# Kernel optimization log

Hardware: AMD Instinct MI355X
Metric: run time of the kernel (lower is better)

## Reference

```python
import jax, jax.numpy as jnp
import numpy as np

EPS_BN = 1e-5      # torch BatchNorm2d default eps
EPSILON = 1e-12    # signed-sqrt eps from the module
K = 3              # hardcoded k in forward


def _knn_idx(f, k):
    # f: [B, C, N] -> idx [B, N, k] of nearest neighbors (largest -dist^2)
    xx = jnp.sum(f * f, axis=1)                      # [B, N]
    inner = jnp.einsum('bcn,bcm->bnm', f, f)         # [B, N, N]
    pd = -xx[:, :, None] + 2.0 * inner - xx[:, None, :]
    return jax.lax.top_k(pd, k)[1]                   # [B, N, k]


def _graph_feature(f, k):
    # f: [B, C, N] -> [B, N, k, 2C] = concat(neighbor - center, center)
    idx = _knn_idx(f, k)
    ft = jnp.transpose(f, (0, 2, 1))                 # [B, N, C]
    neigh = jax.vmap(lambda x, i: x[i])(ft, idx)     # [B, N, k, C]
    center = jnp.broadcast_to(ft[:, :, None, :], neigh.shape)
    return jnp.concatenate([neigh - center, center], axis=-1)


def _edgeconv(f, W, gamma, beta, mean, var, k):
    # f: [B, C, N]; W: [O, 2C] (1x1 conv, no bias); eval-mode BN; LeakyReLU(0.2); max over k
    g = _graph_feature(f, k)                         # [B, N, k, 2C]
    y = jnp.einsum('bnkc,oc->bonk', g, W)            # [B, O, N, k]
    scale = (gamma / jnp.sqrt(var + EPS_BN))[None, :, None, None]
    y = (y - mean[None, :, None, None]) * scale + beta[None, :, None, None]
    y = jnp.where(y >= 0, y, 0.2 * y)                # LeakyReLU(0.2)
    return jnp.max(y, axis=-1)                       # [B, O, N]


def setup_inputs() -> dict:
    key = jax.random.key(0)
    ks = jax.random.split(key, 12)
    B, C, H, W, M = 64, 768, 26, 26, 32
    inp = {
        'features': jax.random.normal(ks[0], (B, C, H, W), jnp.float32),
        'attentions': jax.random.uniform(ks[1], (B, M, H, W), jnp.float32),
        'W1': jax.random.normal(ks[2], (C, 2 * C), jnp.float32) * 0.02,
        'gamma1': jax.random.uniform(ks[3], (C,), jnp.float32, 0.5, 1.5),
        'beta1': jax.random.normal(ks[4], (C,), jnp.float32) * 0.1,
        'mean1': jax.random.normal(ks[5], (C,), jnp.float32) * 0.1,
        'var1': jax.random.uniform(ks[6], (C,), jnp.float32, 0.5, 1.5),
        'W2': jax.random.normal(ks[7], (C, 2 * C), jnp.float32) * 0.02,
        'gamma2': jax.random.uniform(ks[8], (C,), jnp.float32, 0.5, 1.5),
        'beta2': jax.random.normal(ks[9], (C,), jnp.float32) * 0.1,
        'mean2': jax.random.normal(ks[10], (C,), jnp.float32) * 0.1,
        'var2': jax.random.uniform(ks[11], (C,), jnp.float32, 0.5, 1.5),
    }
    return inp


def reference(features, attentions, W1, gamma1, beta1, mean1, var1,
              W2, gamma2, beta2, mean2, var2):
    B = features.shape[0]
    # AdaptiveMaxPool2d(1) of features * attn_m, per attention map m.
    # lax.map over M avoids materializing the [B, M, C, H, W] product.
    def per_m(attn_m):                                # attn_m: [B, H, W]
        return jnp.max(features * attn_m[:, None, :, :], axis=(2, 3))  # [B, C]
    fm = jax.lax.map(per_m, jnp.transpose(attentions, (1, 0, 2, 3)))   # [M, B, C]
    fm = jnp.transpose(fm, (1, 2, 0))                 # [B, C, M]

    f1 = _edgeconv(fm, W1, gamma1, beta1, mean1, var1, K)   # [B, C, M]
    f2 = _edgeconv(f1, W2, gamma2, beta2, mean2, var2, K)   # [B, C, M]

    fuse = jnp.concatenate([f1, f2], axis=1).reshape(B, -1)  # [B, 2C*M]
    fuse = jnp.sign(fuse) * jnp.sqrt(jnp.abs(fuse) + EPSILON)
    norm = jnp.maximum(jnp.linalg.norm(fuse, axis=-1, keepdims=True), 1e-12)
    return fuse / norm
```

## Files before the change

kernel.cpp:

```cpp
#include <hip/hip_runtime.h>
#include <cfloat>
#include <cmath>

#define B_    64
#define C_    768
#define HW_   676
#define M_    32
#define TWOC_ 1536

__global__ __launch_bounds__(256) void pool_kernel(
    const float* __restrict__ feat, const float* __restrict__ attn,
    float* __restrict__ fm)
{
    const int b      = blockIdx.x / 12;
    const int cchunk = blockIdx.x % 12;
    const int t  = threadIdx.x;
    const int cl = t >> 2;
    const int m0 = (t & 3) * 8;
    const int c  = cchunk * 64 + cl;

    __shared__ float a_s[64][32];

    float acc[8];
#pragma unroll
    for (int j = 0; j < 8; ++j) acc[j] = -FLT_MAX;

    const float* fp = feat + ((size_t)b * C_ + c) * HW_;
    const float* ap = attn + (size_t)b * M_ * HW_;

    for (int hw0 = 0; hw0 < HW_; hw0 += 64) {
        const int hwlen = min(64, HW_ - hw0);
        __syncthreads();
        for (int idx = t; idx < 64 * 32; idx += 256) {
            int hw = idx >> 5, m = idx & 31;
            if (hw < hwlen) a_s[hw][m] = ap[m * HW_ + hw0 + hw];
        }
        __syncthreads();
        for (int hw = 0; hw < hwlen; hw += 4) {
            float4 f4 = *(const float4*)(fp + hw0 + hw);
            float fv[4] = {f4.x, f4.y, f4.z, f4.w};
#pragma unroll
            for (int q = 0; q < 4; ++q) {
                float f = fv[q];
#pragma unroll
                for (int j = 0; j < 8; ++j) {
                    float p = __fmul_rn(f, a_s[hw + q][m0 + j]);
                    acc[j] = fmaxf(acc[j], p);
                }
            }
        }
    }
    float* op = fm + ((size_t)b * C_ + c) * M_ + m0;
#pragma unroll
    for (int j = 0; j < 8; ++j) op[j] = acc[j];
}

__global__ __launch_bounds__(1024) void knn_kernel(
    const float* __restrict__ X, int* __restrict__ idxout)
{
    const int b = blockIdx.x;
    const int t = threadIdx.x;
    const int n = t >> 5, m = t & 31;

    __shared__ float xs[96][32];
    __shared__ float GF[32][32];
    __shared__ float G2[32][32];
    __shared__ float XS[32];
    __shared__ float XP[32];
    __shared__ float PA[32][32], PC[32][32], PDm[32][32];

    const float* Xb = X + (size_t)b * (C_ * M_);
    float accF = 0.f;
    float accP0 = 0.f, accP1 = 0.f;
    float accXs = 0.f;
    float leaf[8];

#pragma unroll
    for (int chunk = 0; chunk < 8; ++chunk) {
        __syncthreads();
        for (int i = t; i < 96 * 32; i += 1024)
            xs[i >> 5][i & 31] = Xb[(size_t)(chunk * 96 + (i >> 5)) * M_ + (i & 31)];
        __syncthreads();
#pragma unroll
        for (int c = 0; c < 96; ++c)
            accF = __fmaf_rn(xs[c][n], xs[c][m], accF);
        if (chunk < 4) {
#pragma unroll
            for (int c = 0; c < 96; ++c)
                accP0 = __fmaf_rn(xs[c][n], xs[c][m], accP0);
        } else {
#pragma unroll
            for (int c = 0; c < 96; ++c)
                accP1 = __fmaf_rn(xs[c][n], xs[c][m], accP1);
        }
        if (t < 32) {
#pragma unroll
            for (int c = 0; c < 96; ++c) {
                float v = xs[c][m];
                accXs = __fadd_rn(accXs, __fmul_rn(v, v));
            }
            float r[8];
#pragma unroll
            for (int j = 0; j < 8; ++j) {
                float v = xs[j][m];
                r[j] = __fmul_rn(v, v);
            }
            for (int i = 8; i < 96; i += 8) {
#pragma unroll
                for (int j = 0; j < 8; ++j) {
                    float v = xs[i + j][m];
                    r[j] = __fadd_rn(r[j], __fmul_rn(v, v));
                }
            }
            leaf[chunk] = __fadd_rn(
                __fadd_rn(__fadd_rn(r[0], r[1]), __fadd_rn(r[2], r[3])),
                __fadd_rn(__fadd_rn(r[4], r[5]), __fadd_rn(r[6], r[7])));
        }
    }
    GF[n][m] = accF;
    G2[n][m] = __fadd_rn(accP0, accP1);
    if (t < 32) {
        XS[m] = accXs;
        XP[m] = __fadd_rn(
            __fadd_rn(__fadd_rn(leaf[0], leaf[1]), __fadd_rn(leaf[2], leaf[3])),
            __fadd_rn(__fadd_rn(leaf[4], leaf[5]), __fadd_rn(leaf[6], leaf[7])));
    }
    __syncthreads();
    PA[n][m]  = __fsub_rn(__fadd_rn(-XS[n], 2.0f * GF[n][m]), XS[m]);
    PC[n][m]  = __fsub_rn(__fadd_rn(-XP[n], 2.0f * G2[n][m]), XP[m]);
    PDm[n][m] = __fsub_rn(__fadd_rn(-XP[n], 2.0f * GF[n][m]), XP[m]);
    __syncthreads();

    if (t < 32) {
        const int nn = t;
        const float* pa = PA[nn];
        const float* pc = PC[nn];
        const float* pd = PDm[nn];

        unsigned masks[3] = {0u, 0u, 0u};
        const float* rows[3] = {pa, pc, pd};
#pragma unroll
        for (int s = 0; s < 3; ++s) {
            unsigned chosen = 0;
            for (int p = 0; p < 3; ++p) {
                float best = -FLT_MAX; int bi = 0;
                for (int mm = 0; mm < 32; ++mm) {
                    if (chosen & (1u << mm)) continue;
                    float v = rows[s][mm];
                    if (v > best) { best = v; bi = mm; }
                }
                chosen |= 1u << bi;
            }
            masks[s] = chosen;
        }
        const unsigned mA = masks[0], mC = masks[1], mD = masks[2];

        unsigned chosen = 0;
        for (int p = 0; p < 3; ++p) {
            int bv = -1; float bp = -FLT_MAX; int bi = 0;
            for (int mm = 0; mm < 32; ++mm) {
                if (chosen & (1u << mm)) continue;
                int v = (int)((mA >> mm) & 1u) + (int)((mC >> mm) & 1u)
                      + (int)((mD >> mm) & 1u);
                float q = pd[mm];
                if (v > bv || (v == bv && q > bp)) { bv = v; bp = q; bi = mm; }
            }
            chosen |= 1u << bi;
            idxout[((size_t)b * 32 + nn) * 3 + p] = bi;
        }
    }
}

__global__ __launch_bounds__(256) void conv_kernel(
    const float* __restrict__ X, const float* __restrict__ W,
    const int* __restrict__ idx,
    const float* __restrict__ gamma, const float* __restrict__ beta,
    const float* __restrict__ mean,  const float* __restrict__ var,
    float* __restrict__ fout)
{
    const int b  = blockIdx.x / 12;
    const int oT = blockIdx.x % 12;
    const int o0 = oT * 64;
    const int t  = threadIdx.x;
    const int oG = t >> 4;
    const int nkg = t & 15;

    __shared__ float fs[C_ * M_];
    __shared__ int   idx_s[M_ * 3];

    const float* Xb = X + (size_t)b * (C_ * M_);
    for (int i = t; i < (C_ * M_) / 4; i += 256)
        ((float4*)fs)[i] = ((const float4*)Xb)[i];
    if (t < 96) idx_s[t] = idx[b * 96 + t];
    __syncthreads();

    const int n_0 = nkg * 2;
    int nn_[6], jj[6];
#pragma unroll
    for (int q = 0; q < 6; ++q) {
        nn_[q] = n_0 + (q >= 3 ? 1 : 0);
        jj[q]  = idx_s[nn_[q] * 3 + (q % 3)];
    }

    const float* Wr0 = W + (size_t)(o0 + oG * 4 + 0) * TWOC_;
    const float* Wr1 = W + (size_t)(o0 + oG * 4 + 1) * TWOC_;
    const float* Wr2 = W + (size_t)(o0 + oG * 4 + 2) * TWOC_;
    const float* Wr3 = W + (size_t)(o0 + oG * 4 + 3) * TWOC_;

    float A[4][6], Bv[4][6], Cv[4][6], Dv[4][6];

    auto sweep = [&](int lane, float (&OUT)[4][6]) {
#pragma unroll
        for (int i = 0; i < 4; ++i)
#pragma unroll
            for (int q = 0; q < 6; ++q) OUT[i][q] = 0.f;
        for (int c = lane; c < C_; c += 8) {
            float w0 = Wr0[c], w1 = Wr1[c], w2 = Wr2[c], w3 = Wr3[c];
            float g[6];
#pragma unroll
            for (int q = 0; q < 6; ++q)
                g[q] = __fsub_rn(fs[c * 32 + jj[q]], fs[c * 32 + nn_[q]]);
#pragma unroll
            for (int q = 0; q < 6; ++q) {
                OUT[0][q] = __fmaf_rn(w0, g[q], OUT[0][q]);
                OUT[1][q] = __fmaf_rn(w1, g[q], OUT[1][q]);
                OUT[2][q] = __fmaf_rn(w2, g[q], OUT[2][q]);
                OUT[3][q] = __fmaf_rn(w3, g[q], OUT[3][q]);
            }
        }
        for (int c = C_ + lane; c < TWOC_; c += 8) {
            float w0 = Wr0[c], w1 = Wr1[c], w2 = Wr2[c], w3 = Wr3[c];
            float g[6];
#pragma unroll
            for (int q = 0; q < 6; ++q)
                g[q] = fs[(c - C_) * 32 + nn_[q]];
#pragma unroll
            for (int q = 0; q < 6; ++q) {
                OUT[0][q] = __fmaf_rn(w0, g[q], OUT[0][q]);
                OUT[1][q] = __fmaf_rn(w1, g[q], OUT[1][q]);
                OUT[2][q] = __fmaf_rn(w2, g[q], OUT[2][q]);
                OUT[3][q] = __fmaf_rn(w3, g[q], OUT[3][q]);
            }
        }
    };
    auto add24 = [&](float (&Xa)[4][6], float (&Ya)[4][6]) {
#pragma unroll
        for (int i = 0; i < 4; ++i)
#pragma unroll
            for (int q = 0; q < 6; ++q)
                Xa[i][q] = __fadd_rn(Xa[i][q], Ya[i][q]);
    };

    sweep(0, A);  sweep(4, Bv); add24(A, Bv);
    sweep(2, Bv); sweep(6, Cv); add24(Bv, Cv);
    add24(A, Bv);
    sweep(1, Bv); sweep(5, Cv); add24(Bv, Cv);
    sweep(3, Cv); sweep(7, Dv); add24(Cv, Dv);
    add24(Bv, Cv);
    add24(A, Bv);

#pragma unroll
    for (int i = 0; i < 4; ++i) {
        const int o = o0 + oG * 4 + i;
        const float sc = __fdiv_rn(gamma[o], __fsqrt_rn(__fadd_rn(var[o], 1e-5f)));
        const float mu = mean[o], be = beta[o];
#pragma unroll
        for (int nl = 0; nl < 2; ++nl) {
            float r = -FLT_MAX;
#pragma unroll
            for (int k = 0; k < 3; ++k) {
                float y = A[i][nl * 3 + k];
                y = __fadd_rn(__fmul_rn(__fsub_rn(y, mu), sc), be);
                y = (y >= 0.f) ? y : __fmul_rn(0.2f, y);
                r = fmaxf(r, y);
            }
            fout[((size_t)b * C_ + o) * M_ + (n_0 + nl)] = r;
        }
    }
}

__global__ __launch_bounds__(256) void fuse_kernel(
    const float* __restrict__ f1, const float* __restrict__ f2,
    float* __restrict__ out)
{
    const int b = blockIdx.x;
    const int t = threadIdx.x;
    const float* p1 = f1 + (size_t)b * (C_ * M_);
    const float* p2 = f2 + (size_t)b * (C_ * M_);
    float* po = out + (size_t)b * (2 * C_ * M_);

    __shared__ double red[256];

    double lsum = 0.0;
    for (int i = t; i < 2 * C_ * M_; i += 256) {
        float x = (i < C_ * M_) ? p1[i] : p2[i - C_ * M_];
        float sq = __fsqrt_rn(__fadd_rn(fabsf(x), 1e-12f));
        float s = (x > 0.f) ? sq : ((x < 0.f) ? -sq : 0.f);
        lsum += (double)s * (double)s;
    }
    red[t] = lsum;
    __syncthreads();
    for (int off = 128; off > 0; off >>= 1) {
        if (t < off) red[t] += red[t + off];
        __syncthreads();
    }
    const float normf = fmaxf((float)sqrt(red[0]), 1e-12f);
    for (int i = t; i < 2 * C_ * M_; i += 256) {
        float x = (i < C_ * M_) ? p1[i] : p2[i - C_ * M_];
        float sq = __fsqrt_rn(__fadd_rn(fabsf(x), 1e-12f));
        float s = (x > 0.f) ? sq : ((x < 0.f) ? -sq : 0.f);
        po[i] = __fdiv_rn(s, normf);
    }
}

extern "C" void kernel_launch(void* const* d_in, const int* in_sizes, int n_in,
                              void* d_out, int out_size, void* d_ws, size_t ws_size,
                              hipStream_t stream)
{
    const float* feat = (const float*)d_in[0];
    const float* attn = (const float*)d_in[1];
    const float* W1   = (const float*)d_in[2];
    const float* g1   = (const float*)d_in[3];
    const float* be1  = (const float*)d_in[4];
    const float* mu1  = (const float*)d_in[5];
    const float* va1  = (const float*)d_in[6];
    const float* W2   = (const float*)d_in[7];
    const float* g2   = (const float*)d_in[8];
    const float* be2  = (const float*)d_in[9];
    const float* mu2  = (const float*)d_in[10];
    const float* va2  = (const float*)d_in[11];

    const size_t FM = (size_t)B_ * C_ * M_;
    float* fm  = (float*)d_ws;
    float* f1  = fm + FM;
    float* f2  = f1 + FM;
    int* idx1  = (int*)(f2 + FM);
    int* idx2  = idx1 + B_ * M_ * 3;

    pool_kernel<<<dim3(768), dim3(256), 0, stream>>>(feat, attn, fm);
    knn_kernel<<<dim3(64), dim3(1024), 0, stream>>>(fm, idx1);
    conv_kernel<<<dim3(768), dim3(256), 0, stream>>>(fm, W1, idx1, g1, be1, mu1, va1, f1);
    knn_kernel<<<dim3(64), dim3(1024), 0, stream>>>(f1, idx2);
    conv_kernel<<<dim3(768), dim3(256), 0, stream>>>(f1, W2, idx2, g2, be2, mu2, va2, f2);
    fuse_kernel<<<dim3(64), dim3(256), 0, stream>>>(f1, f2, (float*)d_out);
}
```

Measured before the change: 1.396 ms.

## Map one output channel per thread in conv kernel with 1024-thread blocks

The edge-conv kernel moves from 256-thread blocks, where each thread accumulated four output channels, to 1024-thread blocks where each thread computes a single output channel for its pair of points. Because the 96 KB shared feature tile allows only one block per CU, this raises the number of waves per CU so memory and LDS latency can be hidden better. In exchange, each gathered feature difference read from shared memory now feeds one FMA instead of four. That quadruples LDS traffic per FMA and also multiplies redundant weight loads.

```diff
diff --git a/kernel.cpp b/kernel.cpp
--- a/kernel.cpp
+++ b/kernel.cpp
@@ -171,7 +171,7 @@
     }
 }
 
-__global__ __launch_bounds__(256) void conv_kernel(
+__global__ __launch_bounds__(1024, 4) void conv_kernel(
     const float* __restrict__ X, const float* __restrict__ W,
     const int* __restrict__ idx,
     const float* __restrict__ gamma, const float* __restrict__ beta,
@@ -189,7 +189,7 @@
     __shared__ int   idx_s[M_ * 3];
 
     const float* Xb = X + (size_t)b * (C_ * M_);
-    for (int i = t; i < (C_ * M_) / 4; i += 256)
+    for (int i = t; i < (C_ * M_) / 4; i += 1024)
         ((float4*)fs)[i] = ((const float4*)Xb)[i];
     if (t < 96) idx_s[t] = idx[b * 96 + t];
     __syncthreads();
@@ -202,80 +202,58 @@
         jj[q]  = idx_s[nn_[q] * 3 + (q % 3)];
     }
 
-    const float* Wr0 = W + (size_t)(o0 + oG * 4 + 0) * TWOC_;
-    const float* Wr1 = W + (size_t)(o0 + oG * 4 + 1) * TWOC_;
-    const float* Wr2 = W + (size_t)(o0 + oG * 4 + 2) * TWOC_;
-    const float* Wr3 = W + (size_t)(o0 + oG * 4 + 3) * TWOC_;
-
-    float A[4][6], Bv[4][6], Cv[4][6], Dv[4][6];
-
-    auto sweep = [&](int lane, float (&OUT)[4][6]) {
-#pragma unroll
-        for (int i = 0; i < 4; ++i)
-#pragma unroll
-            for (int q = 0; q < 6; ++q) OUT[i][q] = 0.f;
+    const int o = o0 + oG;
+    const float* Wr = W + (size_t)o * TWOC_;
+
+    float A[6], Bv[6], Cv[6], Dv[6];
+
+    auto sweep = [&](int lane, float (&OUT)[6]) {
+#pragma unroll
+        for (int q = 0; q < 6; ++q) OUT[q] = 0.f;
         for (int c = lane; c < C_; c += 8) {
-            float w0 = Wr0[c], w1 = Wr1[c], w2 = Wr2[c], w3 = Wr3[c];
-            float g[6];
-#pragma unroll
-            for (int q = 0; q < 6; ++q)
-                g[q] = __fsub_rn(fs[c * 32 + jj[q]], fs[c * 32 + nn_[q]]);
+            float w = Wr[c];
 #pragma unroll
             for (int q = 0; q < 6; ++q) {
-                OUT[0][q] = __fmaf_rn(w0, g[q], OUT[0][q]);
-                OUT[1][q] = __fmaf_rn(w1, g[q], OUT[1][q]);
-                OUT[2][q] = __fmaf_rn(w2, g[q], OUT[2][q]);
-                OUT[3][q] = __fmaf_rn(w3, g[q], OUT[3][q]);
+                float g = __fsub_rn(fs[c * 32 + jj[q]], fs[c * 32 + nn_[q]]);
+                OUT[q] = __fmaf_rn(w, g, OUT[q]);
             }
         }
         for (int c = C_ + lane; c < TWOC_; c += 8) {
-            float w0 = Wr0[c], w1 = Wr1[c], w2 = Wr2[c], w3 = Wr3[c];
-            float g[6];
-#pragma unroll
-            for (int q = 0; q < 6; ++q)
-                g[q] = fs[(c - C_) * 32 + nn_[q]];
+            float w = Wr[c];
 #pragma unroll
             for (int q = 0; q < 6; ++q) {
-                OUT[0][q] = __fmaf_rn(w0, g[q], OUT[0][q]);
-                OUT[1][q] = __fmaf_rn(w1, g[q], OUT[1][q]);
-                OUT[2][q] = __fmaf_rn(w2, g[q], OUT[2][q]);
-                OUT[3][q] = __fmaf_rn(w3, g[q], OUT[3][q]);
+                float g = fs[(c - C_) * 32 + nn_[q]];
+                OUT[q] = __fmaf_rn(w, g, OUT[q]);
             }
         }
     };
-    auto add24 = [&](float (&Xa)[4][6], float (&Ya)[4][6]) {
-#pragma unroll
-        for (int i = 0; i < 4; ++i)
-#pragma unroll
-            for (int q = 0; q < 6; ++q)
-                Xa[i][q] = __fadd_rn(Xa[i][q], Ya[i][q]);
+    auto add6 = [&](float (&Xa)[6], float (&Ya)[6]) {
+#pragma unroll
+        for (int q = 0; q < 6; ++q)
+            Xa[q] = __fadd_rn(Xa[q], Ya[q]);
     };
 
-    sweep(0, A);  sweep(4, Bv); add24(A, Bv);
-    sweep(2, Bv); sweep(6, Cv); add24(Bv, Cv);
-    add24(A, Bv);
-    sweep(1, Bv); sweep(5, Cv); add24(Bv, Cv);
-    sweep(3, Cv); sweep(7, Dv); add24(Cv, Dv);
-    add24(Bv, Cv);
-    add24(A, Bv);
-
-#pragma unroll
-    for (int i = 0; i < 4; ++i) {
-        const int o = o0 + oG * 4 + i;
-        const float sc = __fdiv_rn(gamma[o], __fsqrt_rn(__fadd_rn(var[o], 1e-5f)));
-        const float mu = mean[o], be = beta[o];
-#pragma unroll
-        for (int nl = 0; nl < 2; ++nl) {
-            float r = -FLT_MAX;
-#pragma unroll
-            for (int k = 0; k < 3; ++k) {
-                float y = A[i][nl * 3 + k];
-                y = __fadd_rn(__fmul_rn(__fsub_rn(y, mu), sc), be);
-                y = (y >= 0.f) ? y : __fmul_rn(0.2f, y);
-                r = fmaxf(r, y);
-            }
-            fout[((size_t)b * C_ + o) * M_ + (n_0 + nl)] = r;
-        }
+    sweep(0, A);  sweep(4, Bv); add6(A, Bv);
+    sweep(2, Bv); sweep(6, Cv); add6(Bv, Cv);
+    add6(A, Bv);
+    sweep(1, Bv); sweep(5, Cv); add6(Bv, Cv);
+    sweep(3, Cv); sweep(7, Dv); add6(Cv, Dv);
+    add6(Bv, Cv);
+    add6(A, Bv);
+
+    const float sc = __fdiv_rn(gamma[o], __fsqrt_rn(__fadd_rn(var[o], 1e-5f)));
+    const float mu = mean[o], be = beta[o];
+#pragma unroll
+    for (int nl = 0; nl < 2; ++nl) {
+        float r = -FLT_MAX;
+#pragma unroll
+        for (int k = 0; k < 3; ++k) {
+            float y = A[nl * 3 + k];
+            y = __fadd_rn(__fmul_rn(__fsub_rn(y, mu), sc), be);
+            y = (y >= 0.f) ? y : __fmul_rn(0.2f, y);
+            r = fmaxf(r, y);
+        }
+        fout[((size_t)b * C_ + o) * M_ + (n_0 + nl)] = r;
     }
 }
 
@@ -339,8 +317,8 @@
 
     pool_kernel<<<dim3(768), dim3(256), 0, stream>>>(feat, attn, fm);
     knn_kernel<<<dim3(64), dim3(1024), 0, stream>>>(fm, idx1);
-    conv_kernel<<<dim3(768), dim3(256), 0, stream>>>(fm, W1, idx1, g1, be1, mu1, va1, f1);
+    conv_kernel<<<dim3(768), dim3(1024), 0, stream>>>(fm, W1, idx1, g1, be1, mu1, va1, f1);
     knn_kernel<<<dim3(64), dim3(1024), 0, stream>>>(f1, idx2);
-    conv_kernel<<<dim3(768), dim3(256), 0, stream>>>(f1, W2, idx2, g2, be2, mu2, va2, f2);
+    conv_kernel<<<dim3(768), dim3(1024), 0, stream>>>(f1, W2, idx2, g2, be2, mu2, va2, f2);
     fuse_kernel<<<dim3(64), dim3(256), 0, stream>>>(f1, f2, (float*)d_out);
 }
```

Measured after the change: 1.374 ms. Within noise of the previous version (-1.5%).
